# Kernel tuning notes

Hardware: AMD Instinct MI355X
Metric: run time of the kernel (lower is better)

Reference implementation:

```python
import jax, jax.numpy as jnp
import numpy as np

DIM = 512
HEADS = 8
DEPTH = DIM // HEADS
DFF = 2048
EPS = 1e-3  # keras BatchNormalization default epsilon


def _dense_params(key, d_in, d_out, bias=True):
    k1, k2 = jax.random.split(key)
    lim = 1.0 / np.sqrt(d_in)
    W = jax.random.uniform(k1, (d_in, d_out), minval=-lim, maxval=lim, dtype=jnp.float32)
    if bias:
        b = jnp.zeros((d_out,), jnp.float32)
        return W, b
    return W


def _bn_params(key, d):
    k1, k2 = jax.random.split(key)
    gamma = 1.0 + 0.1 * jax.random.normal(k1, (d,), jnp.float32)
    beta = 0.1 * jax.random.normal(k2, (d,), jnp.float32)
    mean = 0.05 * jax.random.normal(jax.random.fold_in(key, 7), (d,), jnp.float32)
    var = jnp.ones((d,), jnp.float32)
    return gamma, beta, mean, var


def setup_inputs() -> dict:
    key = jax.random.key(0)
    ks = jax.random.split(key, 20)
    B, S_dec, S_enc = 32, 384, 384
    inp = {
        'enc_output': jax.random.normal(ks[0], (B, S_enc, DIM), jnp.float32),
        'x2': jax.random.normal(ks[1], (B, S_dec, DIM), jnp.float32),
    }
    # mha1 (self-attn) params
    for i, nm in enumerate(['q1', 'k1', 'v1', 'o1']):
        W, b = _dense_params(ks[2 + i], DIM, DIM)
        inp[f'W{nm}'], inp[f'b{nm}'] = W, b
    # mha2 (cross-attn) params
    for i, nm in enumerate(['q2', 'k2', 'v2', 'o2']):
        W, b = _dense_params(ks[6 + i], DIM, DIM)
        inp[f'W{nm}'], inp[f'b{nm}'] = W, b
    # FFN
    inp['Wff1'] = _dense_params(ks[10], DIM, DFF, bias=False)
    inp['Wff2'] = _dense_params(ks[11], DFF, DIM, bias=False)
    # 4 batchnorms
    for i in range(1, 5):
        g, be, m, v = _bn_params(ks[11 + i], DIM)
        inp[f'bn{i}_gamma'], inp[f'bn{i}_beta'] = g, be
        inp[f'bn{i}_mean'], inp[f'bn{i}_var'] = m, v
    return inp


def _split_heads(x):
    B, S, _ = x.shape
    return x.reshape(B, S, HEADS, DEPTH).transpose(0, 2, 1, 3)


def _mha(q_in, k_in, v_in, Wq, bq, Wk, bk, Wv, bv, Wo, bo, causal):
    q = _split_heads(q_in @ Wq + bq)
    k = _split_heads(k_in @ Wk + bk)
    v = _split_heads(v_in @ Wv + bv)
    logits = jnp.einsum('bhqd,bhkd->bhqk', q, k) / jnp.sqrt(jnp.float32(DEPTH))
    if causal:
        Sq, Sk = logits.shape[-2], logits.shape[-1]
        mask = jnp.tril(jnp.ones((Sq, Sk), bool))
        logits = jnp.where(mask, logits, jnp.finfo(logits.dtype).min)
    attn = jax.nn.softmax(logits, axis=-1)
    out = jnp.einsum('bhqk,bhkd->bhqd', attn, v)
    B, _, S, _ = out.shape
    out = out.transpose(0, 2, 1, 3).reshape(B, S, DIM)
    return out @ Wo + bo


def _bn(x, gamma, beta, mean, var):
    return (x - mean) * jax.lax.rsqrt(var + EPS) * gamma + beta


def reference(enc_output, x2,
              Wq1, bq1, Wk1, bk1, Wv1, bv1, Wo1, bo1,
              Wq2, bq2, Wk2, bk2, Wv2, bv2, Wo2, bo2,
              Wff1, Wff2,
              bn1_gamma, bn1_beta, bn1_mean, bn1_var,
              bn2_gamma, bn2_beta, bn2_mean, bn2_var,
              bn3_gamma, bn3_beta, bn3_mean, bn3_var,
              bn4_gamma, bn4_beta, bn4_mean, bn4_var):
    # self-attention with causal mask (dropout = identity)
    x = _mha(x2, x2, x2, Wq1, bq1, Wk1, bk1, Wv1, bv1, Wo1, bo1, causal=True)
    x = x + x2
    xn = _bn(x, bn1_gamma, bn1_beta, bn1_mean, bn1_var)
    y = _bn(enc_output, bn2_gamma, bn2_beta, bn2_mean, bn2_var)
    # cross-attention (no mask); residual adds x2 (as in source)
    x = _mha(xn, y, y, Wq2, bq2, Wk2, bk2, Wv2, bv2, Wo2, bo2, causal=False)
    x = x + x2
    cross_out = x
    x = _bn(x, bn3_gamma, bn3_beta, bn3_mean, bn3_var)
    x = jax.nn.relu(x @ Wff1) @ Wff2
    x = x + cross_out
    x = _bn(x, bn4_gamma, bn4_beta, bn4_mean, bn4_var)
    return x
```

## Files before the change

### kernel.cpp

```cpp
#include <hip/hip_runtime.h>
#include <cstdint>
#include <cstddef>

typedef __bf16 bf16;
typedef __bf16 bf16x8 __attribute__((ext_vector_type(8)));
typedef __bf16 bf16x4 __attribute__((ext_vector_type(4)));
typedef float  f32x4  __attribute__((ext_vector_type(4)));

#define B_   32
#define S_   384
#define D_   512
#define H_   8
#define DH_  64
#define DFF_ 2048
#define NTOK (B_*S_)

__device__ __forceinline__ void gload16(const void* g, void* l){
  __builtin_amdgcn_global_load_lds((__attribute__((address_space(1))) uint32_t*)(g),
                                   (__attribute__((address_space(3))) uint32_t*)(l), 16, 0, 0);
}

struct Ptr8 { const float* s[8]; };
__global__ __launch_bounds__(256) void transpose_w8(Ptr8 ps, bf16* dst){
  __shared__ float t[64][65];
  int w = blockIdx.z;
  const float* src = ps.s[w];
  bf16* d = dst + (size_t)w*512*512;
  int tr = blockIdx.y*64, tc = blockIdx.x*64;
  for (int i=threadIdx.x; i<4096; i+=256){ int r=i>>6, c=i&63; t[r][c] = src[(size_t)(tr+r)*512 + tc+c]; }
  __syncthreads();
  for (int i=threadIdx.x; i<4096; i+=256){ int c=i>>6, r=i&63; d[(size_t)(tc+c)*512 + tr+r] = (bf16)t[r][c]; }
}

__global__ __launch_bounds__(256) void transpose_rc(const float* __restrict__ src, bf16* __restrict__ dst,
                                                    int R, int C){
  __shared__ float t[64][65];
  int tr = blockIdx.y*64, tc = blockIdx.x*64;
  for (int i=threadIdx.x; i<4096; i+=256){ int r=i>>6, c=i&63; t[r][c] = src[(size_t)(tr+r)*C + tc+c]; }
  __syncthreads();
  for (int i=threadIdx.x; i<4096; i+=256){ int c=i>>6, r=i&63; dst[(size_t)(tc+c)*R + tr+r] = (bf16)t[r][c]; }
}

__global__ __launch_bounds__(256) void transpose_v(const bf16* __restrict__ src, bf16* __restrict__ dst){
  __shared__ bf16 t[64][65];
  int bh = blockIdx.y; int sb = blockIdx.x*64;
  const bf16* s = src + (size_t)bh*S_*DH_;
  bf16* d = dst + (size_t)bh*DH_*S_;
  for (int i=threadIdx.x; i<4096; i+=256){ int r=i>>6, c=i&63; t[r][c] = s[(size_t)(sb+r)*DH_ + c]; }
  __syncthreads();
  for (int i=threadIdx.x; i<4096; i+=256){ int c=i>>6, r=i&63; d[(size_t)c*S_ + sb + r] = t[r][c]; }
}

struct Ptr16 { const float* p[16]; };
__global__ __launch_bounds__(512) void bn_prep(Ptr16 q, float* sc, float* sh){
  int i = blockIdx.x;
  int n = threadIdx.x;
  float g = q.p[i*4+0][n];
  float b = q.p[i*4+1][n];
  float m = q.p[i*4+2][n];
  float v = q.p[i*4+3][n];
  float s = g * rsqrtf(v + 1e-3f);
  sc[i*512+n] = s;
  sh[i*512+n] = b - m*s;
}

__global__ __launch_bounds__(256) void cvt_bn(const float* __restrict__ x, const float* __restrict__ sc,
                                              const float* __restrict__ sh, bf16* __restrict__ out){
  size_t e0 = ((size_t)blockIdx.x*256 + threadIdx.x)*4;
  int n0 = (int)(e0 & (D_-1));
  f32x4 xv = *(const f32x4*)(x + e0);
  bf16x4 ov;
  if (sc){
    #pragma unroll
    for (int j=0;j<4;j++) ov[j] = (bf16)(xv[j]*sc[n0+j] + sh[n0+j]);
  } else {
    #pragma unroll
    for (int j=0;j<4;j++) ov[j] = (bf16)xv[j];
  }
  *(bf16x4*)(out + e0) = ov;
}

__global__ __launch_bounds__(256,4) void gemm_bt(
    const bf16* __restrict__ A, const bf16* __restrict__ Wt,
    const float* __restrict__ b0, const float* __restrict__ b1, const float* __restrict__ b2,
    const float* __restrict__ residf,
    const float* __restrict__ bsc, const float* __restrict__ bsh,
    bf16* __restrict__ o0, bf16* __restrict__ o1b, bf16* __restrict__ o2b,
    float* __restrict__ of, float* __restrict__ o2f,
    int M, int N, int K, int relu, int mode)
{
  __shared__ bf16 As[64*64];
  __shared__ bf16 Bs[128*64];
  int nwg = gridDim.x;
  int cpx = nwg >> 3;
  int bid = blockIdx.x;
  int swz = (bid & 7)*cpx + (bid >> 3);
  int tiles_n = N >> 7;
  int tm = swz / tiles_n, tn = swz - tm*tiles_n;

  int tid = threadIdx.x, wave = tid>>6, lane = tid&63;
  int lhi = lane>>4, llo = lane&15;
  int lrow = lane>>3, lcol = lane&7;
  int wr = wave>>1, wc = wave&1;

  f32x4 acc[2][4];
  #pragma unroll
  for (int i=0;i<2;i++)
    #pragma unroll
    for (int j=0;j<4;j++) acc[i][j] = (f32x4){0.f,0.f,0.f,0.f};

  const bf16* Abase = A  + (size_t)(tm*64)  * K;
  const bf16* Bbase = Wt + (size_t)(tn*128) * K;

  int arow0 = wave*16, brow0 = wave*32;

  for (int kt=0; kt<K; kt+=64){
    #pragma unroll
    for (int q=0;q<2;q++){
      int r = arow0 + q*8 + lrow;
      int s = lcol ^ (r&7);
      gload16(Abase + (size_t)r*K + kt + s*8, (char*)As + wave*2048 + q*1024);
    }
    #pragma unroll
    for (int q=0;q<4;q++){
      int r = brow0 + q*8 + lrow;
      int s = lcol ^ (r&7);
      gload16(Bbase + (size_t)r*K + kt + s*8, (char*)Bs + wave*4096 + q*1024);
    }
    __syncthreads();
    #pragma unroll
    for (int ks=0; ks<2; ks++){
      bf16x8 af[2], bfr[4];
      #pragma unroll
      for (int i=0;i<2;i++){
        int row = wr*32 + i*16 + llo;
        int slot = (ks*4 + lhi) ^ (row&7);
        af[i] = *(const bf16x8*)&As[row*64 + slot*8];
      }
      #pragma unroll
      for (int j=0;j<4;j++){
        int row = wc*64 + j*16 + llo;
        int slot = (ks*4 + lhi) ^ (row&7);
        bfr[j] = *(const bf16x8*)&Bs[row*64 + slot*8];
      }
      #pragma unroll
      for (int i=0;i<2;i++)
        #pragma unroll
        for (int j=0;j<4;j++)
          acc[i][j] = __builtin_amdgcn_mfma_f32_16x16x32_bf16(af[i], bfr[j], acc[i][j], 0,0,0);
    }
    __syncthreads();
  }

  int m0 = tm*64 + wr*32, n0 = tn*128 + wc*64;
  #pragma unroll
  for (int i=0;i<2;i++){
    #pragma unroll
    for (int rr=0;rr<4;rr++){
      int gm = m0 + i*16 + lhi*4 + rr;
      #pragma unroll
      for (int j=0;j<4;j++){
        int gn = n0 + j*16 + llo;
        float v = acc[i][j][rr];
        if (b0){
          const float* bp = (gn < 512) ? b0 : ((gn < 1024) ? b1 : b2);
          v += bp[gn & 511];
        }
        if (residf) v += residf[(size_t)gm*N + gn];
        if (o2f)    o2f[(size_t)gm*N + gn] = v;
        if (bsc)    v = v*bsc[gn & 511] + bsh[gn & 511];
        if (relu)   v = fmaxf(v, 0.f);
        if (mode == 0){
          if (of) of[(size_t)gm*N + gn] = v;
          else    o0[(size_t)gm*N + gn] = (bf16)v;
        } else {
          int seg = gn >> 9;
          bf16* hp = (seg == 0) ? o0 : ((seg == 1) ? o1b : o2b);
          int cn = gn & 511;
          int h = cn >> 6, dd = cn & 63;
          int bb = gm / S_, ss = gm - bb*S_;
          hp[(((size_t)(bb*H_ + h))*S_ + ss)*DH_ + dd] = (bf16)v;
        }
      }
    }
  }
}

__global__ __launch_bounds__(256,4) void attn(
    const bf16* __restrict__ Q, const bf16* __restrict__ Kx,
    const bf16* __restrict__ Vt, bf16* __restrict__ out, int causal)
{
  __shared__ bf16 Ks[64*64];
  __shared__ bf16 Vs[64*64];
  __shared__ bf16 Ps[4][16*64];
  int bid = blockIdx.x;
  int bh = bid & 255;
  int qb = bid >> 8;
  int b = bh >> 3, h = bh & 7;
  int tid = threadIdx.x, wave = tid>>6, lane = tid&63;
  int lhi = lane>>4, llo = lane&15;
  int l7 = llo & 7;
  const bf16* Qb = Q  + (size_t)bh*S_*DH_;
  const bf16* Kb = Kx + (size_t)bh*S_*DH_;
  const bf16* Vb = Vt + (size_t)bh*DH_*S_;

  bf16x8 qf[2];
  #pragma unroll
  for (int f=0; f<2; f++)
    qf[f] = *(const bf16x8*)&Qb[(size_t)(qb*64 + wave*16 + llo)*DH_ + f*32 + lhi*8];

  f32x4 oacc[4];
  #pragma unroll
  for (int f=0; f<4; f++) oacc[f] = (f32x4){0.f,0.f,0.f,0.f};
  float mrow[4], lrow4[4];
  #pragma unroll
  for (int r=0;r<4;r++){ mrow[r] = -1e9f; lrow4[r] = 0.f; }

  int KT = causal ? (qb+1) : (S_/64);

  int srow0 = tid>>3, sslot = tid&7;
  bf16x8 kreg[2], vreg[2];

  auto issue = [&](int kb){
    const bf16* kt0 = Kb + (size_t)kb*64*DH_;
    #pragma unroll
    for (int s=0;s<2;s++){
      int row = s*32 + srow0;
      kreg[s] = *(const bf16x8*)&kt0[(size_t)row*64 + sslot*8];
      vreg[s] = *(const bf16x8*)&Vb[(size_t)row*S_ + (size_t)kb*64 + sslot*8];
    }
  };
  issue(0);

  for (int kb=0; kb<KT; kb++){
    #pragma unroll
    for (int s=0;s<2;s++){
      int row = s*32 + srow0;
      int sl = sslot ^ (row&7);
      *(bf16x8*)&Ks[row*64 + sl*8] = kreg[s];
      *(bf16x8*)&Vs[row*64 + sl*8] = vreg[s];
    }
    __syncthreads();

    f32x4 sc[4];
    #pragma unroll
    for (int f=0; f<4; f++){
      f32x4 z = (f32x4){0.f,0.f,0.f,0.f};
      #pragma unroll
      for (int ks=0; ks<2; ks++){
        int row = f*16 + llo;
        int slot = (ks*4 + lhi) ^ (row&7);
        bf16x8 kf = *(const bf16x8*)&Ks[row*64 + slot*8];
        z = __builtin_amdgcn_mfma_f32_16x16x32_bf16(qf[ks], kf, z, 0,0,0);
      }
      sc[f] = z;
    }
    #pragma unroll
    for (int f=0; f<4; f++)
      #pragma unroll
      for (int r=0;r<4;r++){
        float v = sc[f][r]*0.125f;
        if (causal && kb==KT-1){
          int gcol = kb*64 + f*16 + llo;
          int grow = qb*64 + wave*16 + lhi*4 + r;
          if (gcol > grow) v = -1e9f;
        }
        sc[f][r] = v;
      }

    float alpha[4], psum[4];
    #pragma unroll
    for (int r=0;r<4;r++){
      float vm = fmaxf(fmaxf(sc[0][r],sc[1][r]), fmaxf(sc[2][r],sc[3][r]));
      #pragma unroll
      for (int msk=1; msk<16; msk<<=1) vm = fmaxf(vm, __shfl_xor(vm, msk));
      float mn = fmaxf(mrow[r], vm);
      alpha[r] = __expf(mrow[r]-mn);
      mrow[r]  = mn;
      psum[r]  = 0.f;
    }
    #pragma unroll
    for (int f=0; f<4; f++)
      #pragma unroll
      for (int r=0;r<4;r++){
        float p = __expf(sc[f][r]-mrow[r]);
        psum[r] += p;
        int row = lhi*4 + r;
        int slot = (f*2 + (llo>>3)) ^ (row&7);
        Ps[wave][row*64 + slot*8 + l7] = (bf16)p;
      }
    #pragma unroll
    for (int r=0;r<4;r++){
      float s = psum[r];
      #pragma unroll
      for (int msk=1; msk<16; msk<<=1) s += __shfl_xor(s, msk);
      lrow4[r] = lrow4[r]*alpha[r] + s;
      #pragma unroll
      for (int f=0; f<4; f++) oacc[f][r] *= alpha[r];
    }

    if (kb+1 < KT) issue(kb+1);

    asm volatile("s_waitcnt lgkmcnt(0)" ::: "memory");
    __builtin_amdgcn_sched_barrier(0);

    #pragma unroll
    for (int ks=0; ks<2; ks++){
      int pslot = (ks*4 + lhi) ^ l7;
      bf16x8 pf = *(const bf16x8*)&Ps[wave][llo*64 + pslot*8];
      #pragma unroll
      for (int f2=0; f2<4; f2++){
        int row = f2*16 + llo;
        int slot = (ks*4 + lhi) ^ (row&7);
        bf16x8 vf = *(const bf16x8*)&Vs[row*64 + slot*8];
        oacc[f2] = __builtin_amdgcn_mfma_f32_16x16x32_bf16(pf, vf, oacc[f2], 0,0,0);
      }
    }
    __syncthreads();
  }

  int qg = qb*64 + wave*16;
  #pragma unroll
  for (int f2=0; f2<4; f2++)
    #pragma unroll
    for (int r=0;r<4;r++){
      int row = qg + lhi*4 + r;
      int dd  = f2*16 + llo;
      out[((size_t)(b*S_ + row))*D_ + h*DH_ + dd] = (bf16)(oacc[f2][r] / lrow4[r]);
    }
}

extern "C" void kernel_launch(void* const* d_in, const int* in_sizes, int n_in,
                              void* d_out, int out_size, void* d_ws, size_t ws_size,
                              hipStream_t stream)
{
  (void)in_sizes; (void)n_in; (void)out_size; (void)ws_size;
  const float* enc = (const float*)d_in[0];
  const float* x2  = (const float*)d_in[1];
  const float* Wq1 = (const float*)d_in[2];  const float* bq1 = (const float*)d_in[3];
  const float* Wk1 = (const float*)d_in[4];  const float* bk1 = (const float*)d_in[5];
  const float* Wv1 = (const float*)d_in[6];  const float* bv1 = (const float*)d_in[7];
  const float* Wo1 = (const float*)d_in[8];  const float* bo1 = (const float*)d_in[9];
  const float* Wq2 = (const float*)d_in[10]; const float* bq2 = (const float*)d_in[11];
  const float* Wk2 = (const float*)d_in[12]; const float* bk2 = (const float*)d_in[13];
  const float* Wv2 = (const float*)d_in[14]; const float* bv2 = (const float*)d_in[15];
  const float* Wo2 = (const float*)d_in[16]; const float* bo2 = (const float*)d_in[17];
  const float* Wff1= (const float*)d_in[18]; const float* Wff2= (const float*)d_in[19];
  float* outp = (float*)d_out;

  char* ws = (char*)d_ws;
  size_t off = 0;
  auto alloc = [&](size_t bytes)->void*{ void* p = ws + off; off += (bytes+255)&~(size_t)255; return p; };
  bf16* Wt8   = (bf16*)alloc((size_t)8*512*512*2);
  bf16* Wff1t = (bf16*)alloc((size_t)DFF_*D_*2);
  bf16* Wff2t = (bf16*)alloc((size_t)D_*DFF_*2);
  float* bnsc = (float*)alloc(4*512*4);
  float* bnsh = (float*)alloc(4*512*4);
  size_t actB = (size_t)NTOK*D_*2;
  bf16* X2b  = (bf16*)alloc(actB);
  bf16* Abuf = (bf16*)alloc(actB);
  bf16* Bbuf = (bf16*)alloc(actB);
  bf16* Cbuf = (bf16*)alloc(actB);
  bf16* Dv   = (bf16*)alloc(actB);
  bf16* E1   = (bf16*)alloc(actB);
  bf16* E2   = (bf16*)alloc(actB);
  bf16* Fbuf = Abuf;

  bf16* Wtq1 = Wt8 + 0*262144;
  bf16* Wto1 = Wt8 + 3*262144;
  bf16* Wtq2 = Wt8 + 4*262144;
  bf16* Wtk2 = Wt8 + 5*262144;
  bf16* Wto2 = Wt8 + 7*262144;

  Ptr8 p8;
  p8.s[0]=Wq1; p8.s[1]=Wk1; p8.s[2]=Wv1; p8.s[3]=Wo1;
  p8.s[4]=Wq2; p8.s[5]=Wk2; p8.s[6]=Wv2; p8.s[7]=Wo2;
  transpose_w8<<<dim3(8,8,8),256,0,stream>>>(p8, Wt8);
  transpose_rc<<<dim3(DFF_/64, D_/64),256,0,stream>>>(Wff1, Wff1t, D_, DFF_);
  transpose_rc<<<dim3(D_/64, DFF_/64),256,0,stream>>>(Wff2, Wff2t, DFF_, D_);

  Ptr16 p16;
  for (int i=0;i<16;i++) p16.p[i] = (const float*)d_in[20+i];
  bn_prep<<<4,512,0,stream>>>(p16, bnsc, bnsh);
  int cvtg = NTOK*D_/4/256;
  cvt_bn<<<cvtg,256,0,stream>>>(enc, bnsc+512, bnsh+512, E2);
  cvt_bn<<<cvtg,256,0,stream>>>(x2, nullptr, nullptr, X2b);

  auto gemm = [&](const bf16* Am, const bf16* W,
                  const float* bb0, const float* bb1, const float* bb2,
                  const float* residf, const float* sc, const float* sh,
                  bf16* oo0, bf16* oo1, bf16* oo2, float* of, float* o2f,
                  int N, int K, int relu, int mode){
    gemm_bt<<<(NTOK/64)*(N/128), 256, 0, stream>>>(Am, W, bb0, bb1, bb2, residf, sc, sh,
                                                   oo0, oo1, oo2, of, o2f, NTOK, N, K, relu, mode);
  };

  gemm(X2b, Wtq1, bq1, bk1, bv1, nullptr, nullptr, nullptr,
       Abuf, Bbuf, Cbuf, nullptr, nullptr, 1536, 512, 0, 1);
  transpose_v<<<dim3(S_/64, B_*H_),256,0,stream>>>(Cbuf, Dv);
  attn<<<(S_/64)*B_*H_, 256, 0, stream>>>(Abuf, Bbuf, Dv, Cbuf, 1);
  gemm(Cbuf, Wto1, bo1, nullptr, nullptr, x2, bnsc+0, bnsh+0,
       E1, nullptr, nullptr, nullptr, nullptr, 512, 512, 0, 0);

  gemm(E1, Wtq2, bq2, nullptr, nullptr, nullptr, nullptr, nullptr,
       Abuf, nullptr, nullptr, nullptr, nullptr, 512, 512, 0, 1);
  gemm(E2, Wtk2, bk2, bv2, nullptr, nullptr, nullptr, nullptr,
       Bbuf, Cbuf, nullptr, nullptr, nullptr, 1024, 512, 0, 1);
  transpose_v<<<dim3(S_/64, B_*H_),256,0,stream>>>(Cbuf, Dv);
  attn<<<(S_/64)*B_*H_, 256, 0, stream>>>(Abuf, Bbuf, Dv, Cbuf, 0);
  gemm(Cbuf, Wto2, bo2, nullptr, nullptr, x2, bnsc+2*512, bnsh+2*512,
       E1, nullptr, nullptr, nullptr, outp, 512, 512, 0, 0);

  gemm(E1, Wff1t, nullptr, nullptr, nullptr, nullptr, nullptr, nullptr,
       Fbuf, nullptr, nullptr, nullptr, nullptr, DFF_, 512, 1, 0);
  gemm(Fbuf, Wff2t, nullptr, nullptr, nullptr, outp, bnsc+3*512, bnsh+3*512,
       nullptr, nullptr, nullptr, outp, nullptr, 512, DFF_, 0, 0);
}
```

Measured before the change: 366.4 us.

## Double-buffer GEMM LDS, fuse V transpose into epilogue, use bf16 residuals

The GEMM main loop now uses two LDS buffers so the next K tile is prefetched while MFMAs run on the current one. Occupancy hint drops from 4 to 3 blocks to make room for the extra shared memory. The V projection epilogue writes V already transposed into the per-head layout, which removes both transpose_v launches. Residuals are read as bf16 (X2b, and a bf16 cross_out copy in E3) rather than fp32, cutting epilogue memory traffic at some precision cost. The two input conversion kernels are also merged into one launch.

```diff
diff --git a/kernel.cpp b/kernel.cpp
--- a/kernel.cpp
+++ b/kernel.cpp
@@ -39,16 +39,6 @@
   for (int i=threadIdx.x; i<4096; i+=256){ int r=i>>6, c=i&63; t[r][c] = src[(size_t)(tr+r)*C + tc+c]; }
   __syncthreads();
   for (int i=threadIdx.x; i<4096; i+=256){ int c=i>>6, r=i&63; dst[(size_t)(tc+c)*R + tr+r] = (bf16)t[r][c]; }
-}
-
-__global__ __launch_bounds__(256) void transpose_v(const bf16* __restrict__ src, bf16* __restrict__ dst){
-  __shared__ bf16 t[64][65];
-  int bh = blockIdx.y; int sb = blockIdx.x*64;
-  const bf16* s = src + (size_t)bh*S_*DH_;
-  bf16* d = dst + (size_t)bh*DH_*S_;
-  for (int i=threadIdx.x; i<4096; i+=256){ int r=i>>6, c=i&63; t[r][c] = s[(size_t)(sb+r)*DH_ + c]; }
-  __syncthreads();
-  for (int i=threadIdx.x; i<4096; i+=256){ int c=i>>6, r=i&63; d[(size_t)c*S_ + sb + r] = t[r][c]; }
 }
 
 struct Ptr16 { const float* p[16]; };
@@ -64,33 +54,38 @@
   sh[i*512+n] = b - m*s;
 }
 
-__global__ __launch_bounds__(256) void cvt_bn(const float* __restrict__ x, const float* __restrict__ sc,
-                                              const float* __restrict__ sh, bf16* __restrict__ out){
+__global__ __launch_bounds__(256) void cvt2(const float* __restrict__ enc, const float* __restrict__ x2,
+                                            const float* __restrict__ sc, const float* __restrict__ sh,
+                                            bf16* __restrict__ E2, bf16* __restrict__ X2b){
   size_t e0 = ((size_t)blockIdx.x*256 + threadIdx.x)*4;
-  int n0 = (int)(e0 & (D_-1));
-  f32x4 xv = *(const f32x4*)(x + e0);
-  bf16x4 ov;
-  if (sc){
+  if (blockIdx.y == 0){
+    int n0 = (int)(e0 & (D_-1));
+    f32x4 xv = *(const f32x4*)(enc + e0);
+    bf16x4 ov;
     #pragma unroll
     for (int j=0;j<4;j++) ov[j] = (bf16)(xv[j]*sc[n0+j] + sh[n0+j]);
+    *(bf16x4*)(E2 + e0) = ov;
   } else {
+    f32x4 xv = *(const f32x4*)(x2 + e0);
+    bf16x4 ov;
     #pragma unroll
     for (int j=0;j<4;j++) ov[j] = (bf16)xv[j];
+    *(bf16x4*)(X2b + e0) = ov;
   }
-  *(bf16x4*)(out + e0) = ov;
-}
-
-__global__ __launch_bounds__(256,4) void gemm_bt(
+}
+
+__global__ __launch_bounds__(256,3) void gemm_bt(
     const bf16* __restrict__ A, const bf16* __restrict__ Wt,
     const float* __restrict__ b0, const float* __restrict__ b1, const float* __restrict__ b2,
-    const float* __restrict__ residf,
+    const bf16* __restrict__ residb,
     const float* __restrict__ bsc, const float* __restrict__ bsh,
-    bf16* __restrict__ o0, bf16* __restrict__ o1b, bf16* __restrict__ o2b,
-    float* __restrict__ of, float* __restrict__ o2f,
+    bf16* __restrict__ o0, bf16* __restrict__ o1b,
+    bf16* __restrict__ vt, int vseg,
+    float* __restrict__ of, bf16* __restrict__ pre,
     int M, int N, int K, int relu, int mode)
 {
-  __shared__ bf16 As[64*64];
-  __shared__ bf16 Bs[128*64];
+  __shared__ bf16 As[2][64*64];
+  __shared__ bf16 Bs[2][128*64];
   int nwg = gridDim.x;
   int cpx = nwg >> 3;
   int bid = blockIdx.x;
@@ -114,20 +109,27 @@
 
   int arow0 = wave*16, brow0 = wave*32;
 
-  for (int kt=0; kt<K; kt+=64){
+  auto STAGE = [&](int buf, int kt){
     #pragma unroll
     for (int q=0;q<2;q++){
       int r = arow0 + q*8 + lrow;
       int s = lcol ^ (r&7);
-      gload16(Abase + (size_t)r*K + kt + s*8, (char*)As + wave*2048 + q*1024);
+      gload16(Abase + (size_t)r*K + kt + s*8, (char*)&As[buf][0] + wave*2048 + q*1024);
     }
     #pragma unroll
     for (int q=0;q<4;q++){
       int r = brow0 + q*8 + lrow;
       int s = lcol ^ (r&7);
-      gload16(Bbase + (size_t)r*K + kt + s*8, (char*)Bs + wave*4096 + q*1024);
-    }
-    __syncthreads();
+      gload16(Bbase + (size_t)r*K + kt + s*8, (char*)&Bs[buf][0] + wave*4096 + q*1024);
+    }
+  };
+
+  STAGE(0, 0);
+  __syncthreads();
+  int nt = K >> 6;
+  int cur = 0;
+  for (int t=0; t<nt; ++t){
+    if (t+1 < nt) STAGE(cur^1, (t+1)<<6);
     #pragma unroll
     for (int ks=0; ks<2; ks++){
       bf16x8 af[2], bfr[4];
@@ -135,13 +137,13 @@
       for (int i=0;i<2;i++){
         int row = wr*32 + i*16 + llo;
         int slot = (ks*4 + lhi) ^ (row&7);
-        af[i] = *(const bf16x8*)&As[row*64 + slot*8];
+        af[i] = *(const bf16x8*)&As[cur][row*64 + slot*8];
       }
       #pragma unroll
       for (int j=0;j<4;j++){
         int row = wc*64 + j*16 + llo;
         int slot = (ks*4 + lhi) ^ (row&7);
-        bfr[j] = *(const bf16x8*)&Bs[row*64 + slot*8];
+        bfr[j] = *(const bf16x8*)&Bs[cur][row*64 + slot*8];
       }
       #pragma unroll
       for (int i=0;i<2;i++)
@@ -150,36 +152,53 @@
           acc[i][j] = __builtin_amdgcn_mfma_f32_16x16x32_bf16(af[i], bfr[j], acc[i][j], 0,0,0);
     }
     __syncthreads();
+    cur ^= 1;
   }
 
   int m0 = tm*64 + wr*32, n0 = tn*128 + wc*64;
   #pragma unroll
   for (int i=0;i<2;i++){
     #pragma unroll
-    for (int rr=0;rr<4;rr++){
-      int gm = m0 + i*16 + lhi*4 + rr;
-      #pragma unroll
-      for (int j=0;j<4;j++){
-        int gn = n0 + j*16 + llo;
+    for (int j=0;j<4;j++){
+      int gn = n0 + j*16 + llo;
+      float vv[4];
+      #pragma unroll
+      for (int rr=0;rr<4;rr++){
+        int gm = m0 + i*16 + lhi*4 + rr;
         float v = acc[i][j][rr];
         if (b0){
           const float* bp = (gn < 512) ? b0 : ((gn < 1024) ? b1 : b2);
           v += bp[gn & 511];
         }
-        if (residf) v += residf[(size_t)gm*N + gn];
-        if (o2f)    o2f[(size_t)gm*N + gn] = v;
-        if (bsc)    v = v*bsc[gn & 511] + bsh[gn & 511];
-        if (relu)   v = fmaxf(v, 0.f);
-        if (mode == 0){
+        if (residb) v += (float)residb[(size_t)gm*N + gn];
+        vv[rr] = v;
+      }
+      int gm0 = m0 + i*16 + lhi*4;
+      if (mode == 1){
+        int seg = gn >> 9, cn = gn & 511;
+        int h = cn >> 6, dd = cn & 63;
+        int bb = gm0 / S_, ss0 = gm0 - bb*S_;
+        if (seg == vseg){
+          bf16x4 v4;
+          #pragma unroll
+          for (int rr=0;rr<4;rr++) v4[rr] = (bf16)vv[rr];
+          *(bf16x4*)&vt[((size_t)(bb*H_ + h)*DH_ + dd)*S_ + ss0] = v4;
+        } else {
+          bf16* hp = (seg == 0) ? o0 : o1b;
+          #pragma unroll
+          for (int rr=0;rr<4;rr++)
+            hp[(((size_t)(bb*H_ + h))*S_ + ss0 + rr)*DH_ + dd] = (bf16)vv[rr];
+        }
+      } else {
+        #pragma unroll
+        for (int rr=0;rr<4;rr++){
+          int gm = gm0 + rr;
+          float v = vv[rr];
+          if (pre)  pre[(size_t)gm*N + gn] = (bf16)v;
+          if (bsc)  v = v*bsc[gn & 511] + bsh[gn & 511];
+          if (relu) v = fmaxf(v, 0.f);
           if (of) of[(size_t)gm*N + gn] = v;
           else    o0[(size_t)gm*N + gn] = (bf16)v;
-        } else {
-          int seg = gn >> 9;
-          bf16* hp = (seg == 0) ? o0 : ((seg == 1) ? o1b : o2b);
-          int cn = gn & 511;
-          int h = cn >> 6, dd = cn & 63;
-          int bb = gm / S_, ss = gm - bb*S_;
-          hp[(((size_t)(bb*H_ + h))*S_ + ss)*DH_ + dd] = (bf16)v;
         }
       }
     }
@@ -364,6 +383,7 @@
   bf16* Dv   = (bf16*)alloc(actB);
   bf16* E1   = (bf16*)alloc(actB);
   bf16* E2   = (bf16*)alloc(actB);
+  bf16* E3   = E2;
   bf16* Fbuf = Abuf;
 
   bf16* Wtq1 = Wt8 + 0*262144;
@@ -382,37 +402,35 @@
   Ptr16 p16;
   for (int i=0;i<16;i++) p16.p[i] = (const float*)d_in[20+i];
   bn_prep<<<4,512,0,stream>>>(p16, bnsc, bnsh);
-  int cvtg = NTOK*D_/4/256;
-  cvt_bn<<<cvtg,256,0,stream>>>(enc, bnsc+512, bnsh+512, E2);
-  cvt_bn<<<cvtg,256,0,stream>>>(x2, nullptr, nullptr, X2b);
+  cvt2<<<dim3(NTOK*D_/4/256, 2),256,0,stream>>>(enc, x2, bnsc+512, bnsh+512, E2, X2b);
 
   auto gemm = [&](const bf16* Am, const bf16* W,
                   const float* bb0, const float* bb1, const float* bb2,
-                  const float* residf, const float* sc, const float* sh,
-                  bf16* oo0, bf16* oo1, bf16* oo2, float* of, float* o2f,
+                  const bf16* residb, const float* sc, const float* sh,
+                  bf16* oo0, bf16* oo1, bf16* vt, int vseg,
+                  float* of, bf16* pre,
                   int N, int K, int relu, int mode){
-    gemm_bt<<<(NTOK/64)*(N/128), 256, 0, stream>>>(Am, W, bb0, bb1, bb2, residf, sc, sh,
-                                                   oo0, oo1, oo2, of, o2f, NTOK, N, K, relu, mode);
+    gemm_bt<<<(NTOK/64)*(N/128), 256, 0, stream>>>(Am, W, bb0, bb1, bb2, residb, sc, sh,
+                                                   oo0, oo1, vt, vseg, of, pre,
+                                                   NTOK, N, K, relu, mode);
   };
 
   gemm(X2b, Wtq1, bq1, bk1, bv1, nullptr, nullptr, nullptr,
-       Abuf, Bbuf, Cbuf, nullptr, nullptr, 1536, 512, 0, 1);
-  transpose_v<<<dim3(S_/64, B_*H_),256,0,stream>>>(Cbuf, Dv);
+       Abuf, Bbuf, Dv, 2, nullptr, nullptr, 1536, 512, 0, 1);
   attn<<<(S_/64)*B_*H_, 256, 0, stream>>>(Abuf, Bbuf, Dv, Cbuf, 1);
-  gemm(Cbuf, Wto1, bo1, nullptr, nullptr, x2, bnsc+0, bnsh+0,
-       E1, nullptr, nullptr, nullptr, nullptr, 512, 512, 0, 0);
+  gemm(Cbuf, Wto1, bo1, nullptr, nullptr, X2b, bnsc+0, bnsh+0,
+       E1, nullptr, nullptr, -1, nullptr, nullptr, 512, 512, 0, 0);
 
   gemm(E1, Wtq2, bq2, nullptr, nullptr, nullptr, nullptr, nullptr,
-       Abuf, nullptr, nullptr, nullptr, nullptr, 512, 512, 0, 1);
+       Abuf, nullptr, nullptr, -1, nullptr, nullptr, 512, 512, 0, 1);
   gemm(E2, Wtk2, bk2, bv2, nullptr, nullptr, nullptr, nullptr,
-       Bbuf, Cbuf, nullptr, nullptr, nullptr, 1024, 512, 0, 1);
-  transpose_v<<<dim3(S_/64, B_*H_),256,0,stream>>>(Cbuf, Dv);
+       Bbuf, nullptr, Dv, 1, nullptr, nullptr, 1024, 512, 0, 1);
   attn<<<(S_/64)*B_*H_, 256, 0, stream>>>(Abuf, Bbuf, Dv, Cbuf, 0);
-  gemm(Cbuf, Wto2, bo2, nullptr, nullptr, x2, bnsc+2*512, bnsh+2*512,
-       E1, nullptr, nullptr, nullptr, outp, 512, 512, 0, 0);
+  gemm(Cbuf, Wto2, bo2, nullptr, nullptr, X2b, bnsc+2*512, bnsh+2*512,
+       E1, nullptr, nullptr, -1, nullptr, E3, 512, 512, 0, 0);
 
   gemm(E1, Wff1t, nullptr, nullptr, nullptr, nullptr, nullptr, nullptr,
-       Fbuf, nullptr, nullptr, nullptr, nullptr, DFF_, 512, 1, 0);
-  gemm(Fbuf, Wff2t, nullptr, nullptr, nullptr, outp, bnsc+3*512, bnsh+3*512,
-       nullptr, nullptr, nullptr, outp, nullptr, 512, DFF_, 0, 0);
-}
+       Fbuf, nullptr, nullptr, -1, nullptr, nullptr, DFF_, 512, 1, 0);
+  gemm(Fbuf, Wff2t, nullptr, nullptr, nullptr, E3, bnsc+3*512, bnsh+3*512,
+       nullptr, nullptr, nullptr, -1, outp, nullptr, 512, DFF_, 0, 0);
+}
```

Measured after the change: 332.3 us. 1.1x faster.
